# Optimization experiments

Hardware: AMD Instinct MI355X
Metric: run time of the kernel (lower is better)

The kernel has to match this reference:

```python
import jax, jax.numpy as jnp
import numpy as np

N_NODES = 100000
N_RELS = 4
N_EDGES = 200000
D_IN = 256
D_OUT = 256
N_BASES = 2
LN_EPS = 1e-5


def setup_inputs() -> dict:
    key = jax.random.key(0)
    ks = jax.random.split(key, 8)
    x = jax.random.normal(ks[0], (N_NODES, D_IN), dtype=jnp.float32)
    src_idx = jax.random.randint(ks[1], (N_RELS, N_EDGES), 0, N_NODES, dtype=jnp.int32)
    dst_idx = jax.random.randint(ks[2], (N_RELS, N_EDGES), 0, N_NODES, dtype=jnp.int32)
    # WeightBasis: bases [B, in, out], per-relation coefficients [R, B]
    xav = float(np.sqrt(2.0)) * float(np.sqrt(6.0 / (D_IN + D_OUT)))
    bases = jax.random.uniform(ks[3], (N_BASES, D_IN, D_OUT), minval=-xav, maxval=xav, dtype=jnp.float32)
    w_comp = jax.random.normal(ks[4], (N_RELS, N_BASES), dtype=jnp.float32) * 0.5
    loop_weight = jax.random.uniform(ks[5], (D_IN, D_OUT), minval=-xav, maxval=xav, dtype=jnp.float32)
    h_bias = jnp.zeros((D_OUT,), dtype=jnp.float32)
    ln_gamma = jnp.ones((D_OUT,), dtype=jnp.float32)
    ln_beta = jnp.zeros((D_OUT,), dtype=jnp.float32)
    return {"x": x, "src_idx": src_idx, "dst_idx": dst_idx, "bases": bases,
            "w_comp": w_comp, "loop_weight": loop_weight, "h_bias": h_bias,
            "ln_gamma": ln_gamma, "ln_beta": ln_beta}


def reference(x, src_idx, dst_idx, bases, w_comp, loop_weight, h_bias, ln_gamma, ln_beta):
    n = x.shape[0]
    # basis combination -> per-relation weights [R, in, out]
    W = jnp.einsum('rb,bio->rio', w_comp, bases)

    def per_rel(W_r, s, d):
        # GraphConv(norm='right', weight=W_r): aggregate src feats to dst,
        # normalize by in-degree (clamped to 1), then matmul.
        msgs = x[s]                                            # [E, in]
        agg = jax.ops.segment_sum(msgs, d, num_segments=n)     # [N, in]
        deg = jax.ops.segment_sum(jnp.ones(d.shape, x.dtype), d, num_segments=n)
        agg = agg / jnp.maximum(deg, 1.0)[:, None]
        return agg @ W_r                                        # [N, out]

    hs = jax.vmap(per_rel)(W, src_idx, dst_idx).sum(axis=0)    # HeteroGraphConv sum aggregate
    # self-loop + bias
    h = hs + x @ loop_weight + h_bias
    # layer norm
    mu = jnp.mean(h, axis=-1, keepdims=True)
    var = jnp.mean(jnp.square(h - mu), axis=-1, keepdims=True)
    h = (h - mu) * jax.lax.rsqrt(var + LN_EPS) * ln_gamma + ln_beta
    # activation (dropout inactive in eval; NGNN has 0 layers)
    return jax.nn.relu(h)
```

## Files before the change

### kernel.cpp

```cpp
#include <hip/hip_runtime.h>


#define NN 100000
#define NR 4
#define NE 200000
#define KDIM 768
#define CAP 32
#define BM 128

typedef __attribute__((ext_vector_type(8))) short short8;
typedef __attribute__((ext_vector_type(16))) float floatx16;

__device__ __forceinline__ unsigned short f2bf(float f) {
  unsigned u = __float_as_uint(f);
  u += 0x7FFFu + ((u >> 16) & 1u);
  return (unsigned short)(u >> 16);
}

__device__ __forceinline__ void gload16(const unsigned short* g, unsigned short* l) {
  __builtin_amdgcn_global_load_lds(
      (const __attribute__((address_space(1))) unsigned int*)g,
      (__attribute__((address_space(3))) unsigned int*)l, 16, 0, 0);
}

__global__ void prep(const float* __restrict__ x, const float* __restrict__ bases,
                     const float* __restrict__ loop_w, const int* __restrict__ src,
                     const int* __restrict__ dst, unsigned short* __restrict__ A,
                     unsigned short* __restrict__ Bt, int* __restrict__ cnt,
                     int* __restrict__ edgebuf) {
  const int b = blockIdx.x;
  const int tid = threadIdx.x;
  if (b < 3125) {
    int base = b * 256 + tid;
#pragma unroll
    for (int p = 0; p < 4; ++p) {
      int c = base + p * 800000;
      int row = c >> 5;
      int off = (c & 31) << 3;
      const float4 v0 = *(const float4*)(x + (size_t)row * 256 + off);
      const float4 v1 = *(const float4*)(x + (size_t)row * 256 + off + 4);
      uint4 u;
      u.x = (unsigned)f2bf(v0.x) | ((unsigned)f2bf(v0.y) << 16);
      u.y = (unsigned)f2bf(v0.z) | ((unsigned)f2bf(v0.w) << 16);
      u.z = (unsigned)f2bf(v1.x) | ((unsigned)f2bf(v1.y) << 16);
      u.w = (unsigned)f2bf(v1.z) | ((unsigned)f2bf(v1.w) << 16);
      *(uint4*)(A + (size_t)row * KDIM + 512 + off) = u;
    }
  } else if (b < 3893) {
    int i = (b - 3125) * 256 + tid;
    int n = i & 255;
    int k = i >> 8;
    float v;
    if (k < 256)      v = bases[k * 256 + n];
    else if (k < 512) v = bases[65536 + (k - 256) * 256 + n];
    else              v = loop_w[(k - 512) * 256 + n];
    Bt[(size_t)n * KDIM + k] = f2bf(v);
  } else {
    int i = (b - 3893) * 256 + tid;
    int r = i / NE;
    int s = src[i];
    int dd = dst[i];
    int pos = atomicAdd(&cnt[dd], 1);
    if (pos < CAP) edgebuf[dd * CAP + pos] = s | (r << 20);
  }
}

__global__ void agg_edges(const int* __restrict__ edgebuf, const int* __restrict__ cnt,
                          const float* __restrict__ w_comp, unsigned short* __restrict__ A) {
  const int tid = threadIdx.x;
  const int lane = tid & 63;
  const int wave = tid >> 6;
  const int half = lane >> 5;
  const int l31 = lane & 31;
  const int d = blockIdx.x * 8 + wave * 2 + half;

  int cc = cnt[d]; cc = cc < CAP ? cc : CAP;
  int ev = 0;
  if (l31 < cc) ev = edgebuf[d * CAP + l31];
  const int rl = ev >> 20;

  unsigned long long b0 = __ballot((l31 < cc) && rl == 0);
  unsigned long long b1 = __ballot((l31 < cc) && rl == 1);
  unsigned long long b2 = __ballot((l31 < cc) && rl == 2);
  unsigned long long b3 = __ballot((l31 < cc) && rl == 3);
  const int sh = half << 5;
  float i0 = 1.0f / fmaxf((float)__popc((unsigned)(b0 >> sh)), 1.0f);
  float i1 = 1.0f / fmaxf((float)__popc((unsigned)(b1 >> sh)), 1.0f);
  float i2 = 1.0f / fmaxf((float)__popc((unsigned)(b2 >> sh)), 1.0f);
  float i3 = 1.0f / fmaxf((float)__popc((unsigned)(b3 >> sh)), 1.0f);
  float s00 = w_comp[0] * i0, s10 = w_comp[1] * i0;
  float s01 = w_comp[2] * i1, s11 = w_comp[3] * i1;
  float s02 = w_comp[4] * i2, s12 = w_comp[5] * i2;
  float s03 = w_comp[6] * i3, s13 = w_comp[7] * i3;

  float a0[8] = {0.f, 0.f, 0.f, 0.f, 0.f, 0.f, 0.f, 0.f};
  float a1[8] = {0.f, 0.f, 0.f, 0.f, 0.f, 0.f, 0.f, 0.f};
  const unsigned short* Xp = A + 512 + l31 * 8;
  const int selbase = lane & 32;

#define EDGE_W(v, w0, w1)                                            \
  int r_##w0 = (v) >> 20;                                            \
  float w0 = r_##w0 < 2 ? (r_##w0 == 0 ? s00 : s01)                  \
                        : (r_##w0 == 2 ? s02 : s03);                 \
  float w1 = r_##w0 < 2 ? (r_##w0 == 0 ? s10 : s11)                  \
                        : (r_##w0 == 2 ? s12 : s13);

#define ACC8(g, w0, w1)                                              \
  {                                                                  \
    float e0 = __uint_as_float((g).x << 16);                         \
    float e1 = __uint_as_float((g).x & 0xFFFF0000u);                 \
    float e2 = __uint_as_float((g).y << 16);                         \
    float e3 = __uint_as_float((g).y & 0xFFFF0000u);                 \
    float e4 = __uint_as_float((g).z << 16);                         \
    float e5 = __uint_as_float((g).z & 0xFFFF0000u);                 \
    float e6 = __uint_as_float((g).w << 16);                         \
    float e7 = __uint_as_float((g).w & 0xFFFF0000u);                 \
    a0[0] += (w0) * e0; a0[1] += (w0) * e1; a0[2] += (w0) * e2;      \
    a0[3] += (w0) * e3; a0[4] += (w0) * e4; a0[5] += (w0) * e5;      \
    a0[6] += (w0) * e6; a0[7] += (w0) * e7;                          \
    a1[0] += (w1) * e0; a1[1] += (w1) * e1; a1[2] += (w1) * e2;      \
    a1[3] += (w1) * e3; a1[4] += (w1) * e4; a1[5] += (w1) * e5;      \
    a1[6] += (w1) * e6; a1[7] += (w1) * e7;                          \
  }

  int i = 0;
  for (; i + 4 <= cc; i += 4) {
    int v0 = __shfl(ev, selbase + i);
    int v1 = __shfl(ev, selbase + i + 1);
    int v2 = __shfl(ev, selbase + i + 2);
    int v3 = __shfl(ev, selbase + i + 3);
    const uint4 g0 = *(const uint4*)(Xp + (size_t)(v0 & 0xFFFFF) * KDIM);
    const uint4 g1 = *(const uint4*)(Xp + (size_t)(v1 & 0xFFFFF) * KDIM);
    const uint4 g2 = *(const uint4*)(Xp + (size_t)(v2 & 0xFFFFF) * KDIM);
    const uint4 g3 = *(const uint4*)(Xp + (size_t)(v3 & 0xFFFFF) * KDIM);
    { EDGE_W(v0, w0a, w1a) ACC8(g0, w0a, w1a) }
    { EDGE_W(v1, w0b, w1b) ACC8(g1, w0b, w1b) }
    { EDGE_W(v2, w0c, w1c) ACC8(g2, w0c, w1c) }
    { EDGE_W(v3, w0d, w1d) ACC8(g3, w0d, w1d) }
  }
  for (; i < cc; ++i) {
    int v = __shfl(ev, selbase + i);
    const uint4 g = *(const uint4*)(Xp + (size_t)(v & 0xFFFFF) * KDIM);
    EDGE_W(v, w0, w1)
    ACC8(g, w0, w1)
  }

  uint4 o0, o1;
  o0.x = (unsigned)f2bf(a0[0]) | ((unsigned)f2bf(a0[1]) << 16);
  o0.y = (unsigned)f2bf(a0[2]) | ((unsigned)f2bf(a0[3]) << 16);
  o0.z = (unsigned)f2bf(a0[4]) | ((unsigned)f2bf(a0[5]) << 16);
  o0.w = (unsigned)f2bf(a0[6]) | ((unsigned)f2bf(a0[7]) << 16);
  o1.x = (unsigned)f2bf(a1[0]) | ((unsigned)f2bf(a1[1]) << 16);
  o1.y = (unsigned)f2bf(a1[2]) | ((unsigned)f2bf(a1[3]) << 16);
  o1.z = (unsigned)f2bf(a1[4]) | ((unsigned)f2bf(a1[5]) << 16);
  o1.w = (unsigned)f2bf(a1[6]) | ((unsigned)f2bf(a1[7]) << 16);
  *(uint4*)(A + (size_t)d * KDIM + l31 * 8) = o0;
  *(uint4*)(A + (size_t)d * KDIM + 256 + l31 * 8) = o1;
}

__launch_bounds__(256, 2)
__global__ void gemm_ln(const unsigned short* __restrict__ A, const unsigned short* __restrict__ Bt,
                        const float* __restrict__ h_bias, const float* __restrict__ gamma,
                        const float* __restrict__ beta, float* __restrict__ out) {
  __shared__ unsigned short Bs[64 * 512];
  const int tid = threadIdx.x;
  const int wave = tid >> 6;
  const int lane = tid & 63;
  const int l31 = lane & 31;
  const int half = lane >> 5;
  const int m0 = blockIdx.x * BM;

  floatx16 acc[8];
#pragma unroll
  for (int t = 0; t < 8; ++t)
#pragma unroll
    for (int r = 0; r < 16; ++r) acc[t][r] = 0.0f;

  int arow = m0 + wave * 32 + l31;
  if (arow >= NN) arow = NN - 1;
  const unsigned short* gA = A + (size_t)arow * KDIM + half * 8;

#define STAGE_B(s)                                                        \
  {                                                                       \
    const int kb = (s) * 128;                                             \
    _Pragma("unroll")                                                     \
    for (int q = 0; q < 16; ++q) {                                        \
      const int t = wave * 2 + (q >> 3);                                  \
      const int j = q & 7;                                                \
      gload16(Bt + (size_t)(t * 32 + l31) * KDIM + kb + j * 16 + half * 8,\
              Bs + (t * 8 + j) * 512 + lane * 8);                         \
    }                                                                     \
  }

  short8 ab[2][8];
#pragma unroll
  for (int j = 0; j < 8; ++j) ab[0][j] = *(const short8*)(gA + j * 16);
  STAGE_B(0)
  __syncthreads();

#pragma unroll
  for (int s = 0; s < 6; ++s) {
    const int cur = s & 1;
    if (s < 5) {
#pragma unroll
      for (int j = 0; j < 8; ++j)
        ab[cur ^ 1][j] = *(const short8*)(gA + (s + 1) * 128 + j * 16);
    }
#pragma unroll
    for (int j = 0; j < 8; ++j) {
      short8 af = ab[cur][j];
#pragma unroll
      for (int t = 0; t < 8; ++t) {
        short8 bfr = *(const short8*)(Bs + (t * 8 + j) * 512 + lane * 8);
        acc[t] = __builtin_amdgcn_mfma_f32_32x32x16_bf16(af, bfr, acc[t], 0, 0, 0);
      }
    }
    if (s < 5) {
      __syncthreads();
      STAGE_B(s + 1)
      __syncthreads();
    }
  }

  float bcol[8], gc[8], bc[8];
#pragma unroll
  for (int t = 0; t < 8; ++t) {
    int col = t * 32 + l31;
    bcol[t] = h_bias[col];
    gc[t] = gamma[col];
    bc[t] = beta[col];
  }
#pragma unroll
  for (int t = 0; t < 8; ++t)
#pragma unroll
    for (int r = 0; r < 16; ++r) acc[t][r] += bcol[t];

  const int m_base = m0 + wave * 32;
#pragma unroll
  for (int r = 0; r < 16; ++r) {
    float s = 0.f, q = 0.f;
#pragma unroll
    for (int t = 0; t < 8; ++t) { float v = acc[t][r]; s += v; q += v * v; }
#pragma unroll
    for (int m = 16; m >= 1; m >>= 1) {
      s += __shfl_xor(s, m);
      q += __shfl_xor(q, m);
    }
    float mean = s * (1.0f / 256.0f);
    float var = q * (1.0f / 256.0f) - mean * mean;
    float rstd = rsqrtf(var + 1e-5f);
    int row = (r & 3) + ((r >> 2) << 3) + (half << 2);
    int grow = m_base + row;
    if (grow < NN) {
#pragma unroll
      for (int t = 0; t < 8; ++t) {
        float v = (acc[t][r] - mean) * rstd * gc[t] + bc[t];
        out[(size_t)grow * 256 + t * 32 + l31] = fmaxf(v, 0.0f);
      }
    }
  }
}

extern "C" void kernel_launch(void* const* d_in, const int* in_sizes, int n_in,
                              void* d_out, int out_size, void* d_ws, size_t ws_size,
                              hipStream_t stream) {
  const float* x      = (const float*)d_in[0];
  const int*   src    = (const int*)d_in[1];
  const int*   dst    = (const int*)d_in[2];
  const float* bases  = (const float*)d_in[3];
  const float* w_comp = (const float*)d_in[4];
  const float* loop_w = (const float*)d_in[5];
  const float* h_bias = (const float*)d_in[6];
  const float* gamma  = (const float*)d_in[7];
  const float* beta   = (const float*)d_in[8];
  float* out = (float*)d_out;

  char* ws = (char*)d_ws;
  unsigned short* A  = (unsigned short*)ws;
  unsigned short* Bt = (unsigned short*)(ws + 153600000);
  int* cnt     = (int*)(ws + 153993216);
  int* edgebuf = (int*)(ws + 154393216);

  hipMemsetAsync(cnt, 0, 400000, stream);

  prep<<<7018, 256, 0, stream>>>(x, bases, loop_w, src, dst, A, Bt, cnt, edgebuf);
  agg_edges<<<12500, 256, 0, stream>>>(edgebuf, cnt, w_comp, A);
  gemm_ln<<<(NN + BM - 1) / BM, 256, 0, stream>>>(A, Bt, h_bias, gamma, beta, out);
}
```

Measured before the change: 417.0 us.

## Drop bf16 copy of x; gather fp32 x directly and convert in GEMM

The separate pass that converted x to bf16 into the A buffer is removed. The aggregation kernel now gathers fp32 x rows directly, and the GEMM loads fp32 x for the self-loop K-slice, packing it to bf16 in registers with a perm-based rounding. This removes a 100 MB read and 51 MB write pass and shrinks A to 512 columns. The cost is that the random gathers now move twice as many bytes, and the GEMM reads 4-byte x instead of 2-byte values, with extra register pressure from the xr buffers.

After: 467.3 us. 12.1% more time.

```diff
diff --git a/kernel.cpp b/kernel.cpp
--- a/kernel.cpp
+++ b/kernel.cpp
@@ -17,37 +17,33 @@
   return (unsigned short)(u >> 16);
 }
 
+__device__ __forceinline__ short8 packbf(float4 a, float4 b) {
+  union { unsigned u[4]; short8 s; } r;
+  r.u[0] = __builtin_amdgcn_perm(__float_as_uint(a.y) + 0x8000u,
+                                 __float_as_uint(a.x) + 0x8000u, 0x07060302u);
+  r.u[1] = __builtin_amdgcn_perm(__float_as_uint(a.w) + 0x8000u,
+                                 __float_as_uint(a.z) + 0x8000u, 0x07060302u);
+  r.u[2] = __builtin_amdgcn_perm(__float_as_uint(b.y) + 0x8000u,
+                                 __float_as_uint(b.x) + 0x8000u, 0x07060302u);
+  r.u[3] = __builtin_amdgcn_perm(__float_as_uint(b.w) + 0x8000u,
+                                 __float_as_uint(b.z) + 0x8000u, 0x07060302u);
+  return r.s;
+}
+
 __device__ __forceinline__ void gload16(const unsigned short* g, unsigned short* l) {
   __builtin_amdgcn_global_load_lds(
       (const __attribute__((address_space(1))) unsigned int*)g,
       (__attribute__((address_space(3))) unsigned int*)l, 16, 0, 0);
 }
 
-__global__ void prep(const float* __restrict__ x, const float* __restrict__ bases,
-                     const float* __restrict__ loop_w, const int* __restrict__ src,
-                     const int* __restrict__ dst, unsigned short* __restrict__ A,
+__global__ void prep(const float* __restrict__ bases, const float* __restrict__ loop_w,
+                     const int* __restrict__ src, const int* __restrict__ dst,
                      unsigned short* __restrict__ Bt, int* __restrict__ cnt,
                      int* __restrict__ edgebuf) {
   const int b = blockIdx.x;
   const int tid = threadIdx.x;
-  if (b < 3125) {
-    int base = b * 256 + tid;
-#pragma unroll
-    for (int p = 0; p < 4; ++p) {
-      int c = base + p * 800000;
-      int row = c >> 5;
-      int off = (c & 31) << 3;
-      const float4 v0 = *(const float4*)(x + (size_t)row * 256 + off);
-      const float4 v1 = *(const float4*)(x + (size_t)row * 256 + off + 4);
-      uint4 u;
-      u.x = (unsigned)f2bf(v0.x) | ((unsigned)f2bf(v0.y) << 16);
-      u.y = (unsigned)f2bf(v0.z) | ((unsigned)f2bf(v0.w) << 16);
-      u.z = (unsigned)f2bf(v1.x) | ((unsigned)f2bf(v1.y) << 16);
-      u.w = (unsigned)f2bf(v1.z) | ((unsigned)f2bf(v1.w) << 16);
-      *(uint4*)(A + (size_t)row * KDIM + 512 + off) = u;
-    }
-  } else if (b < 3893) {
-    int i = (b - 3125) * 256 + tid;
+  if (b < 768) {
+    int i = b * 256 + tid;
     int n = i & 255;
     int k = i >> 8;
     float v;
@@ -56,7 +52,7 @@
     else              v = loop_w[(k - 512) * 256 + n];
     Bt[(size_t)n * KDIM + k] = f2bf(v);
   } else {
-    int i = (b - 3893) * 256 + tid;
+    int i = (b - 768) * 256 + tid;
     int r = i / NE;
     int s = src[i];
     int dd = dst[i];
@@ -66,7 +62,8 @@
 }
 
 __global__ void agg_edges(const int* __restrict__ edgebuf, const int* __restrict__ cnt,
-                          const float* __restrict__ w_comp, unsigned short* __restrict__ A) {
+                          const float* __restrict__ w_comp, const float* __restrict__ x,
+                          unsigned short* __restrict__ A) {
   const int tid = threadIdx.x;
   const int lane = tid & 63;
   const int wave = tid >> 6;
@@ -95,7 +92,7 @@
 
   float a0[8] = {0.f, 0.f, 0.f, 0.f, 0.f, 0.f, 0.f, 0.f};
   float a1[8] = {0.f, 0.f, 0.f, 0.f, 0.f, 0.f, 0.f, 0.f};
-  const unsigned short* Xp = A + 512 + l31 * 8;
+  const float* Xp = x + l31 * 8;
   const int selbase = lane & 32;
 
 #define EDGE_W(v, w0, w1)                                            \
@@ -105,22 +102,16 @@
   float w1 = r_##w0 < 2 ? (r_##w0 == 0 ? s10 : s11)                  \
                         : (r_##w0 == 2 ? s12 : s13);
 
-#define ACC8(g, w0, w1)                                              \
+#define ACC8(lo, hi, w0, w1)                                         \
   {                                                                  \
-    float e0 = __uint_as_float((g).x << 16);                         \
-    float e1 = __uint_as_float((g).x & 0xFFFF0000u);                 \
-    float e2 = __uint_as_float((g).y << 16);                         \
-    float e3 = __uint_as_float((g).y & 0xFFFF0000u);                 \
-    float e4 = __uint_as_float((g).z << 16);                         \
-    float e5 = __uint_as_float((g).z & 0xFFFF0000u);                 \
-    float e6 = __uint_as_float((g).w << 16);                         \
-    float e7 = __uint_as_float((g).w & 0xFFFF0000u);                 \
-    a0[0] += (w0) * e0; a0[1] += (w0) * e1; a0[2] += (w0) * e2;      \
-    a0[3] += (w0) * e3; a0[4] += (w0) * e4; a0[5] += (w0) * e5;      \
-    a0[6] += (w0) * e6; a0[7] += (w0) * e7;                          \
-    a1[0] += (w1) * e0; a1[1] += (w1) * e1; a1[2] += (w1) * e2;      \
-    a1[3] += (w1) * e3; a1[4] += (w1) * e4; a1[5] += (w1) * e5;      \
-    a1[6] += (w1) * e6; a1[7] += (w1) * e7;                          \
+    a0[0] += (w0) * (lo).x; a0[1] += (w0) * (lo).y;                  \
+    a0[2] += (w0) * (lo).z; a0[3] += (w0) * (lo).w;                  \
+    a0[4] += (w0) * (hi).x; a0[5] += (w0) * (hi).y;                  \
+    a0[6] += (w0) * (hi).z; a0[7] += (w0) * (hi).w;                  \
+    a1[0] += (w1) * (lo).x; a1[1] += (w1) * (lo).y;                  \
+    a1[2] += (w1) * (lo).z; a1[3] += (w1) * (lo).w;                  \
+    a1[4] += (w1) * (hi).x; a1[5] += (w1) * (hi).y;                  \
+    a1[6] += (w1) * (hi).z; a1[7] += (w1) * (hi).w;                  \
   }
 
   int i = 0;
@@ -129,20 +120,25 @@
     int v1 = __shfl(ev, selbase + i + 1);
     int v2 = __shfl(ev, selbase + i + 2);
     int v3 = __shfl(ev, selbase + i + 3);
-    const uint4 g0 = *(const uint4*)(Xp + (size_t)(v0 & 0xFFFFF) * KDIM);
-    const uint4 g1 = *(const uint4*)(Xp + (size_t)(v1 & 0xFFFFF) * KDIM);
-    const uint4 g2 = *(const uint4*)(Xp + (size_t)(v2 & 0xFFFFF) * KDIM);
-    const uint4 g3 = *(const uint4*)(Xp + (size_t)(v3 & 0xFFFFF) * KDIM);
-    { EDGE_W(v0, w0a, w1a) ACC8(g0, w0a, w1a) }
-    { EDGE_W(v1, w0b, w1b) ACC8(g1, w0b, w1b) }
-    { EDGE_W(v2, w0c, w1c) ACC8(g2, w0c, w1c) }
-    { EDGE_W(v3, w0d, w1d) ACC8(g3, w0d, w1d) }
+    const float* p0 = Xp + (size_t)(v0 & 0xFFFFF) * 256;
+    const float* p1 = Xp + (size_t)(v1 & 0xFFFFF) * 256;
+    const float* p2 = Xp + (size_t)(v2 & 0xFFFFF) * 256;
+    const float* p3 = Xp + (size_t)(v3 & 0xFFFFF) * 256;
+    const float4 g0l = *(const float4*)p0, g0h = *(const float4*)(p0 + 4);
+    const float4 g1l = *(const float4*)p1, g1h = *(const float4*)(p1 + 4);
+    const float4 g2l = *(const float4*)p2, g2h = *(const float4*)(p2 + 4);
+    const float4 g3l = *(const float4*)p3, g3h = *(const float4*)(p3 + 4);
+    { EDGE_W(v0, w0a, w1a) ACC8(g0l, g0h, w0a, w1a) }
+    { EDGE_W(v1, w0b, w1b) ACC8(g1l, g1h, w0b, w1b) }
+    { EDGE_W(v2, w0c, w1c) ACC8(g2l, g2h, w0c, w1c) }
+    { EDGE_W(v3, w0d, w1d) ACC8(g3l, g3h, w0d, w1d) }
   }
   for (; i < cc; ++i) {
     int v = __shfl(ev, selbase + i);
-    const uint4 g = *(const uint4*)(Xp + (size_t)(v & 0xFFFFF) * KDIM);
+    const float* p = Xp + (size_t)(v & 0xFFFFF) * 256;
+    const float4 gl = *(const float4*)p, gh = *(const float4*)(p + 4);
     EDGE_W(v, w0, w1)
-    ACC8(g, w0, w1)
+    ACC8(gl, gh, w0, w1)
   }
 
   uint4 o0, o1;
@@ -154,12 +150,13 @@
   o1.y = (unsigned)f2bf(a1[2]) | ((unsigned)f2bf(a1[3]) << 16);
   o1.z = (unsigned)f2bf(a1[4]) | ((unsigned)f2bf(a1[5]) << 16);
   o1.w = (unsigned)f2bf(a1[6]) | ((unsigned)f2bf(a1[7]) << 16);
-  *(uint4*)(A + (size_t)d * KDIM + l31 * 8) = o0;
-  *(uint4*)(A + (size_t)d * KDIM + 256 + l31 * 8) = o1;
+  *(uint4*)(A + (size_t)d * 512 + l31 * 8) = o0;
+  *(uint4*)(A + (size_t)d * 512 + 256 + l31 * 8) = o1;
 }
 
 __launch_bounds__(256, 2)
-__global__ void gemm_ln(const unsigned short* __restrict__ A, const unsigned short* __restrict__ Bt,
+__global__ void gemm_ln(const unsigned short* __restrict__ A, const float* __restrict__ x,
+                        const unsigned short* __restrict__ Bt,
                         const float* __restrict__ h_bias, const float* __restrict__ gamma,
                         const float* __restrict__ beta, float* __restrict__ out) {
   __shared__ unsigned short Bs[64 * 512];
@@ -178,7 +175,8 @@
 
   int arow = m0 + wave * 32 + l31;
   if (arow >= NN) arow = NN - 1;
-  const unsigned short* gA = A + (size_t)arow * KDIM + half * 8;
+  const unsigned short* gA = A + (size_t)arow * 512 + half * 8;
+  const float* gX = x + (size_t)arow * 256 + half * 8;
 
 #define STAGE_B(s)                                                        \
   {                                                                       \
@@ -193,18 +191,25 @@
   }
 
   short8 ab[2][8];
+  float4 xr[8][2];
 #pragma unroll
   for (int j = 0; j < 8; ++j) ab[0][j] = *(const short8*)(gA + j * 16);
   STAGE_B(0)
   __syncthreads();
 
 #pragma unroll
-  for (int s = 0; s < 6; ++s) {
+  for (int s = 0; s < 4; ++s) {
     const int cur = s & 1;
-    if (s < 5) {
+    if (s < 3) {
 #pragma unroll
       for (int j = 0; j < 8; ++j)
         ab[cur ^ 1][j] = *(const short8*)(gA + (s + 1) * 128 + j * 16);
+    } else {
+#pragma unroll
+      for (int j = 0; j < 8; ++j) {
+        xr[j][0] = *(const float4*)(gX + j * 16);
+        xr[j][1] = *(const float4*)(gX + j * 16 + 4);
+      }
     }
 #pragma unroll
     for (int j = 0; j < 8; ++j) {
@@ -215,9 +220,30 @@
         acc[t] = __builtin_amdgcn_mfma_f32_32x32x16_bf16(af, bfr, acc[t], 0, 0, 0);
       }
     }
-    if (s < 5) {
+    __syncthreads();
+    STAGE_B(s + 1)
+    __syncthreads();
+  }
+
+#pragma unroll
+  for (int s = 4; s < 6; ++s) {
+#pragma unroll
+    for (int j = 0; j < 8; ++j) {
+      short8 af = packbf(xr[j][0], xr[j][1]);
+#pragma unroll
+      for (int t = 0; t < 8; ++t) {
+        short8 bfr = *(const short8*)(Bs + (t * 8 + j) * 512 + lane * 8);
+        acc[t] = __builtin_amdgcn_mfma_f32_32x32x16_bf16(af, bfr, acc[t], 0, 0, 0);
+      }
+    }
+    if (s == 4) {
+#pragma unroll
+      for (int j = 0; j < 8; ++j) {
+        xr[j][0] = *(const float4*)(gX + 128 + j * 16);
+        xr[j][1] = *(const float4*)(gX + 128 + j * 16 + 4);
+      }
       __syncthreads();
-      STAGE_B(s + 1)
+      STAGE_B(5)
       __syncthreads();
     }
   }
@@ -277,13 +303,13 @@
 
   char* ws = (char*)d_ws;
   unsigned short* A  = (unsigned short*)ws;
-  unsigned short* Bt = (unsigned short*)(ws + 153600000);
-  int* cnt     = (int*)(ws + 153993216);
-  int* edgebuf = (int*)(ws + 154393216);
+  unsigned short* Bt = (unsigned short*)(ws + 102400000);
+  int* cnt     = (int*)(ws + 102793216);
+  int* edgebuf = (int*)(ws + 103193216);
 
   hipMemsetAsync(cnt, 0, 400000, stream);
 
-  prep<<<7018, 256, 0, stream>>>(x, bases, loop_w, src, dst, A, Bt, cnt, edgebuf);
-  agg_edges<<<12500, 256, 0, stream>>>(edgebuf, cnt, w_comp, A);
-  gemm_ln<<<(NN + BM - 1) / BM, 256, 0, stream>>>(A, Bt, h_bias, gamma, beta, out);
-}
+  prep<<<3893, 256, 0, stream>>>(bases, loop_w, src, dst, Bt, cnt, edgebuf);
+  agg_edges<<<12500, 256, 0, stream>>>(edgebuf, cnt, w_comp, x, A);
+  gemm_ln<<<(NN + BM - 1) / BM, 256, 0, stream>>>(A, x, Bt, h_bias, gamma, beta, out);
+}
```

## Store B in MFMA fragment order and read it directly from global memory

Applied to the files above, without the earlier changes.

The weight matrix is now pre-permuted into per-lane MFMA fragment order, so the GEMM loads B fragments straight from global memory (L2-cached) with register double-buffering. This removes the LDS staging and both __syncthreads barriers from every K stage. The single interleaved A buffer is also split into a compact bf16 X array and a separate aggregated buffer, which shrinks the row stride of the gather in agg_edges. The trade-off is that every wave now rereads B through the cache hierarchy instead of sharing it through LDS, which raises global load traffic and register pressure.

Result: slower. 432.8 us (+3.8%).

```diff
diff --git a/kernel.cpp b/kernel.cpp
--- a/kernel.cpp
+++ b/kernel.cpp
@@ -4,7 +4,6 @@
 #define NN 100000
 #define NR 4
 #define NE 200000
-#define KDIM 768
 #define CAP 32
 #define BM 128
 
@@ -17,46 +16,42 @@
   return (unsigned short)(u >> 16);
 }
 
-__device__ __forceinline__ void gload16(const unsigned short* g, unsigned short* l) {
-  __builtin_amdgcn_global_load_lds(
-      (const __attribute__((address_space(1))) unsigned int*)g,
-      (__attribute__((address_space(3))) unsigned int*)l, 16, 0, 0);
-}
-
 __global__ void prep(const float* __restrict__ x, const float* __restrict__ bases,
                      const float* __restrict__ loop_w, const int* __restrict__ src,
-                     const int* __restrict__ dst, unsigned short* __restrict__ A,
-                     unsigned short* __restrict__ Bt, int* __restrict__ cnt,
+                     const int* __restrict__ dst, unsigned short* __restrict__ Xbf,
+                     unsigned short* __restrict__ Bfrag, int* __restrict__ cnt,
                      int* __restrict__ edgebuf) {
   const int b = blockIdx.x;
   const int tid = threadIdx.x;
-  if (b < 3125) {
-    int base = b * 256 + tid;
-#pragma unroll
-    for (int p = 0; p < 4; ++p) {
-      int c = base + p * 800000;
-      int row = c >> 5;
-      int off = (c & 31) << 3;
-      const float4 v0 = *(const float4*)(x + (size_t)row * 256 + off);
-      const float4 v1 = *(const float4*)(x + (size_t)row * 256 + off + 4);
-      uint4 u;
-      u.x = (unsigned)f2bf(v0.x) | ((unsigned)f2bf(v0.y) << 16);
-      u.y = (unsigned)f2bf(v0.z) | ((unsigned)f2bf(v0.w) << 16);
-      u.z = (unsigned)f2bf(v1.x) | ((unsigned)f2bf(v1.y) << 16);
-      u.w = (unsigned)f2bf(v1.z) | ((unsigned)f2bf(v1.w) << 16);
-      *(uint4*)(A + (size_t)row * KDIM + 512 + off) = u;
-    }
-  } else if (b < 3893) {
-    int i = (b - 3125) * 256 + tid;
-    int n = i & 255;
-    int k = i >> 8;
+  if (b < 12500) {
+    int i = b * 256 + tid;
+    int row = i >> 5;
+    int col = (i & 31) << 3;
+    const float4 v0 = *(const float4*)(x + (size_t)row * 256 + col);
+    const float4 v1 = *(const float4*)(x + (size_t)row * 256 + col + 4);
+    uint4 u;
+    u.x = (unsigned)f2bf(v0.x) | ((unsigned)f2bf(v0.y) << 16);
+    u.y = (unsigned)f2bf(v0.z) | ((unsigned)f2bf(v0.w) << 16);
+    u.z = (unsigned)f2bf(v1.x) | ((unsigned)f2bf(v1.y) << 16);
+    u.w = (unsigned)f2bf(v1.z) | ((unsigned)f2bf(v1.w) << 16);
+    *(uint4*)(Xbf + (size_t)row * 256 + col) = u;
+  } else if (b < 13268) {
+    int i = (b - 12500) * 256 + tid;
+    int e = i & 7;
+    int lane = (i >> 3) & 63;
+    int f = i >> 9;
+    int t = f & 7;
+    int j = (f >> 3) & 7;
+    int s = f >> 6;
+    int n = t * 32 + (lane & 31);
+    int k = s * 128 + j * 16 + (lane >> 5) * 8 + e;
     float v;
     if (k < 256)      v = bases[k * 256 + n];
     else if (k < 512) v = bases[65536 + (k - 256) * 256 + n];
     else              v = loop_w[(k - 512) * 256 + n];
-    Bt[(size_t)n * KDIM + k] = f2bf(v);
+    Bfrag[i] = f2bf(v);
   } else {
-    int i = (b - 3893) * 256 + tid;
+    int i = (b - 13268) * 256 + tid;
     int r = i / NE;
     int s = src[i];
     int dd = dst[i];
@@ -66,7 +61,9 @@
 }
 
 __global__ void agg_edges(const int* __restrict__ edgebuf, const int* __restrict__ cnt,
-                          const float* __restrict__ w_comp, unsigned short* __restrict__ A) {
+                          const float* __restrict__ w_comp,
+                          const unsigned short* __restrict__ Xbf,
+                          unsigned short* __restrict__ Cp) {
   const int tid = threadIdx.x;
   const int lane = tid & 63;
   const int wave = tid >> 6;
@@ -95,7 +92,7 @@
 
   float a0[8] = {0.f, 0.f, 0.f, 0.f, 0.f, 0.f, 0.f, 0.f};
   float a1[8] = {0.f, 0.f, 0.f, 0.f, 0.f, 0.f, 0.f, 0.f};
-  const unsigned short* Xp = A + 512 + l31 * 8;
+  const unsigned short* Xp = Xbf + l31 * 8;
   const int selbase = lane & 32;
 
 #define EDGE_W(v, w0, w1)                                            \
@@ -129,10 +126,10 @@
     int v1 = __shfl(ev, selbase + i + 1);
     int v2 = __shfl(ev, selbase + i + 2);
     int v3 = __shfl(ev, selbase + i + 3);
-    const uint4 g0 = *(const uint4*)(Xp + (size_t)(v0 & 0xFFFFF) * KDIM);
-    const uint4 g1 = *(const uint4*)(Xp + (size_t)(v1 & 0xFFFFF) * KDIM);
-    const uint4 g2 = *(const uint4*)(Xp + (size_t)(v2 & 0xFFFFF) * KDIM);
-    const uint4 g3 = *(const uint4*)(Xp + (size_t)(v3 & 0xFFFFF) * KDIM);
+    const uint4 g0 = *(const uint4*)(Xp + (size_t)(v0 & 0xFFFFF) * 256);
+    const uint4 g1 = *(const uint4*)(Xp + (size_t)(v1 & 0xFFFFF) * 256);
+    const uint4 g2 = *(const uint4*)(Xp + (size_t)(v2 & 0xFFFFF) * 256);
+    const uint4 g3 = *(const uint4*)(Xp + (size_t)(v3 & 0xFFFFF) * 256);
     { EDGE_W(v0, w0a, w1a) ACC8(g0, w0a, w1a) }
     { EDGE_W(v1, w0b, w1b) ACC8(g1, w0b, w1b) }
     { EDGE_W(v2, w0c, w1c) ACC8(g2, w0c, w1c) }
@@ -140,7 +137,7 @@
   }
   for (; i < cc; ++i) {
     int v = __shfl(ev, selbase + i);
-    const uint4 g = *(const uint4*)(Xp + (size_t)(v & 0xFFFFF) * KDIM);
+    const uint4 g = *(const uint4*)(Xp + (size_t)(v & 0xFFFFF) * 256);
     EDGE_W(v, w0, w1)
     ACC8(g, w0, w1)
   }
@@ -154,15 +151,16 @@
   o1.y = (unsigned)f2bf(a1[2]) | ((unsigned)f2bf(a1[3]) << 16);
   o1.z = (unsigned)f2bf(a1[4]) | ((unsigned)f2bf(a1[5]) << 16);
   o1.w = (unsigned)f2bf(a1[6]) | ((unsigned)f2bf(a1[7]) << 16);
-  *(uint4*)(A + (size_t)d * KDIM + l31 * 8) = o0;
-  *(uint4*)(A + (size_t)d * KDIM + 256 + l31 * 8) = o1;
+  *(uint4*)(Cp + (size_t)d * 512 + l31 * 8) = o0;
+  *(uint4*)(Cp + (size_t)d * 512 + 256 + l31 * 8) = o1;
 }
 
 __launch_bounds__(256, 2)
-__global__ void gemm_ln(const unsigned short* __restrict__ A, const unsigned short* __restrict__ Bt,
+__global__ void gemm_ln(const unsigned short* __restrict__ Cp,
+                        const unsigned short* __restrict__ Xbf,
+                        const unsigned short* __restrict__ Bfrag,
                         const float* __restrict__ h_bias, const float* __restrict__ gamma,
                         const float* __restrict__ beta, float* __restrict__ out) {
-  __shared__ unsigned short Bs[64 * 512];
   const int tid = threadIdx.x;
   const int wave = tid >> 6;
   const int lane = tid & 63;
@@ -178,47 +176,42 @@
 
   int arow = m0 + wave * 32 + l31;
   if (arow >= NN) arow = NN - 1;
-  const unsigned short* gA = A + (size_t)arow * KDIM + half * 8;
-
-#define STAGE_B(s)                                                        \
-  {                                                                       \
-    const int kb = (s) * 128;                                             \
-    _Pragma("unroll")                                                     \
-    for (int q = 0; q < 16; ++q) {                                        \
-      const int t = wave * 2 + (q >> 3);                                  \
-      const int j = q & 7;                                                \
-      gload16(Bt + (size_t)(t * 32 + l31) * KDIM + kb + j * 16 + half * 8,\
-              Bs + (t * 8 + j) * 512 + lane * 8);                         \
-    }                                                                     \
-  }
-
-  short8 ab[2][8];
-#pragma unroll
-  for (int j = 0; j < 8; ++j) ab[0][j] = *(const short8*)(gA + j * 16);
-  STAGE_B(0)
-  __syncthreads();
+  const unsigned short* gC = Cp + (size_t)arow * 512 + half * 8;
+  const unsigned short* gX = Xbf + (size_t)arow * 256 + half * 8;
+  const unsigned short* gB = Bfrag + lane * 8;
+
+  short8 Af[2][8];
+  short8 Bf[2][8];
+
+#pragma unroll
+  for (int j = 0; j < 8; ++j) Af[0][j] = *(const short8*)(gC + j * 16);
+#pragma unroll
+  for (int t = 0; t < 8; ++t) Bf[0][t] = *(const short8*)(gB + t * 512);
 
 #pragma unroll
   for (int s = 0; s < 6; ++s) {
-    const int cur = s & 1;
     if (s < 5) {
+      const unsigned short* ap =
+          (s + 1 < 4) ? gC + (s + 1) * 128 : gX + (s + 1 - 4) * 128;
 #pragma unroll
       for (int j = 0; j < 8; ++j)
-        ab[cur ^ 1][j] = *(const short8*)(gA + (s + 1) * 128 + j * 16);
+        Af[(s + 1) & 1][j] = *(const short8*)(ap + j * 16);
     }
 #pragma unroll
     for (int j = 0; j < 8; ++j) {
-      short8 af = ab[cur][j];
-#pragma unroll
-      for (int t = 0; t < 8; ++t) {
-        short8 bfr = *(const short8*)(Bs + (t * 8 + j) * 512 + lane * 8);
-        acc[t] = __builtin_amdgcn_mfma_f32_32x32x16_bf16(af, bfr, acc[t], 0, 0, 0);
+      const int cur = j & 1;
+      if (!(s == 5 && j == 7)) {
+        const int ns = (j == 7) ? s + 1 : s;
+        const int nj = (j + 1) & 7;
+        const unsigned short* bp = gB + (size_t)(ns * 8 + nj) * 8 * 512;
+#pragma unroll
+        for (int t = 0; t < 8; ++t)
+          Bf[cur ^ 1][t] = *(const short8*)(bp + t * 512);
       }
-    }
-    if (s < 5) {
-      __syncthreads();
-      STAGE_B(s + 1)
-      __syncthreads();
+      short8 af = Af[s & 1][j];
+#pragma unroll
+      for (int t = 0; t < 8; ++t)
+        acc[t] = __builtin_amdgcn_mfma_f32_32x32x16_bf16(af, Bf[cur][t], acc[t], 0, 0, 0);
     }
   }
 
@@ -276,14 +269,15 @@
   float* out = (float*)d_out;
 
   char* ws = (char*)d_ws;
-  unsigned short* A  = (unsigned short*)ws;
-  unsigned short* Bt = (unsigned short*)(ws + 153600000);
+  unsigned short* Cp    = (unsigned short*)ws;
+  unsigned short* Xbf   = (unsigned short*)(ws + 102400000);
+  unsigned short* Bfrag = (unsigned short*)(ws + 153600000);
   int* cnt     = (int*)(ws + 153993216);
   int* edgebuf = (int*)(ws + 154393216);
 
   hipMemsetAsync(cnt, 0, 400000, stream);
 
-  prep<<<7018, 256, 0, stream>>>(x, bases, loop_w, src, dst, A, Bt, cnt, edgebuf);
-  agg_edges<<<12500, 256, 0, stream>>>(edgebuf, cnt, w_comp, A);
-  gemm_ln<<<(NN + BM - 1) / BM, 256, 0, stream>>>(A, Bt, h_bias, gamma, beta, out);
-}
+  prep<<<16393, 256, 0, stream>>>(x, bases, loop_w, src, dst, Xbf, Bfrag, cnt, edgebuf);
+  agg_edges<<<12500, 256, 0, stream>>>(edgebuf, cnt, w_comp, Xbf, Cp);
+  gemm_ln<<<(NN + BM - 1) / BM, 256, 0, stream>>>(Cp, Xbf, Bfrag, h_bias, gamma, beta, out);
+}
```
